# Kernel optimization log

Hardware: AMD Instinct MI355X
Metric: run time of the kernel (lower is better)

## Reference

```python
import jax, jax.numpy as jnp
import numpy as np

HEADS = 16

def setup_inputs() -> dict:
    key = jax.random.key(0)
    ks = jax.random.split(key, 5)
    B, N, D = 2, 2048, 1024
    q = jax.random.normal(ks[0], (B, N, D), dtype=jnp.float32)
    kv = jax.random.normal(ks[1], (B, N, D), dtype=jnp.float32)
    # nn.Linear default init scale ~ 1/sqrt(fan_in); use scaled normals
    s = 1.0 / np.sqrt(D)
    Wq = jax.random.normal(ks[2], (D, D), dtype=jnp.float32) * s
    Wkv = jax.random.normal(ks[3], (D, 2 * D), dtype=jnp.float32) * s
    Wout = jax.random.normal(ks[4], (D, D), dtype=jnp.float32) * s
    return {"q": q, "kv": kv, "Wq": Wq, "Wkv": Wkv, "Wout": Wout}

def reference(q, kv, Wq, Wkv, Wout):
    B, N, D = q.shape
    H = HEADS
    Dh = D // H
    scale = Dh ** -0.5
    # projections (Linear, no bias); weights stored [in, out]
    qp = q @ Wq                      # [B,N,D]
    kvp = kv @ Wkv                   # [B,N,2D]
    kp, vp = kvp[..., :D], kvp[..., D:]
    def split_heads(t):
        return t.reshape(B, N, H, Dh).transpose(0, 2, 1, 3)  # [B,H,N,Dh]
    qh, kh, vh = split_heads(qp), split_heads(kp), split_heads(vp)
    dots = jnp.einsum('bhid,bhjd->bhij', qh, kh) * scale
    # attn_fn = softmax computed in float32, cast back to input dtype
    attn = jax.nn.softmax(dots.astype(jnp.float32), axis=-1).astype(dots.dtype)
    out = jnp.einsum('bhij,bhjd->bhid', attn, vh)
    out = out.transpose(0, 2, 1, 3).reshape(B, N, D)
    return out @ Wout
```

## Files before the change

### kernel.cpp

```cpp
#include <hip/hip_runtime.h>
#include <hip/hip_bf16.h>
#include <stdint.h>

using u16 = unsigned short;
using bf16x8 = __attribute__((ext_vector_type(8))) short;
using bf16x4 = __attribute__((ext_vector_type(4))) short;
using f32x4  = __attribute__((ext_vector_type(4))) float;

__device__ __forceinline__ u16 f2bf(float f) {
  union { float f; uint32_t u; } v; v.f = f;
  uint32_t u = v.u;
  u += 0x7fffu + ((u >> 16) & 1u);
  return (u16)(u >> 16);
}

#define GLOBAL_LOAD_LDS16(gp, lp) \
  __builtin_amdgcn_global_load_lds((const __attribute__((address_space(1))) unsigned int*)(gp), \
                                   (__attribute__((address_space(3))) unsigned int*)(lp), 16, 0, 0)

#define MFMA32(a, b, c) __builtin_amdgcn_mfma_f32_16x16x32_bf16(a, b, c, 0, 0, 0)
#define MFMA16(a, b, c) __builtin_amdgcn_mfma_f32_16x16x16bf16_1k(a, b, c, 0, 0, 0)

__global__ __launch_bounds__(256) void cast2_k(const float4* __restrict__ q,
                                               u16* __restrict__ q16,
                                               const float4* __restrict__ kv,
                                               u16* __restrict__ kv16) {
  int blk = blockIdx.x;
  const float4* in; u16* out; int i;
  if (blk < 4096) { in = q; out = q16; i = blk * 256 + threadIdx.x; }
  else { in = kv; out = kv16; i = (blk - 4096) * 256 + threadIdx.x; }
  float4 f = in[i];
  ushort4 o;
  o.x = f2bf(f.x); o.y = f2bf(f.y); o.z = f2bf(f.z); o.w = f2bf(f.w);
  *(ushort4*)(out + (size_t)i * 4) = o;
}

__global__ __launch_bounds__(256) void prep_w_k(const float* __restrict__ Wq,
                                                const float* __restrict__ Wkv,
                                                const float* __restrict__ Wout,
                                                u16* __restrict__ WqT, u16* __restrict__ WkvT,
                                                u16* __restrict__ WoutT, float qscale) {
  __shared__ float tile[32][33];
  int blk = blockIdx.x;
  const float* in; u16* out; float sc; int idx;
  if (blk < 1024)      { in = Wq;   out = WqT;   sc = qscale; idx = blk; }
  else if (blk < 3072) { in = Wkv;  out = WkvT;  sc = 1.0f;   idx = blk - 1024; }
  else                 { in = Wout; out = WoutT; sc = 1.0f;   idx = blk - 3072; }
  const int K = 1024;
  const int N = (blk >= 1024 && blk < 3072) ? 2048 : 1024;
  int bk = (idx & 31) * 32, bn = (idx >> 5) * 32;
  int tx = threadIdx.x & 31, ty = threadIdx.x >> 5;
#pragma unroll
  for (int i = 0; i < 4; i++) {
    int r = ty * 4 + i;
    tile[r][tx] = in[(size_t)(bk + r) * N + bn + tx];
  }
  __syncthreads();
#pragma unroll
  for (int i = 0; i < 4; i++) {
    int r = ty * 4 + i;
    out[(size_t)(bn + r) * K + bk + tx] = f2bf(tile[tx][r] * sc);
  }
}

template <int BM, bool OUT_F32>
__device__ __forceinline__ void gemm_body(u16* lA, u16* lB,
                                          const u16* __restrict__ A, const u16* __restrict__ BT,
                                          void* __restrict__ Cv, int N, int K, int bm, int bn) {
  const int tid = threadIdx.x;
  const int lane = tid & 63, wave = tid >> 6;
  const int l15 = lane & 15, quad = lane >> 4;
  constexpr int MI = BM / 32;
  const int wm = (wave >> 1) * (BM / 2), wn = (wave & 1) * 64;

  f32x4 acc[MI][4] = {};

  const u16* Abase = A + (size_t)bm * BM * K;
  const u16* Bbase = BT + (size_t)bn * 128 * K;
  const int r0 = tid >> 2, c8 = (tid & 3) * 8;

  u16* lAw = lA + wave * 512;
  u16* lBw = lB + wave * 512;

  for (int k0 = 0; k0 < K; k0 += 32) {
    const u16* Ag = Abase + k0 + (size_t)r0 * K + c8;
    const u16* Bg = Bbase + k0 + (size_t)r0 * K + c8;
#pragma unroll
    for (int t = 0; t < BM / 64; t++)
      GLOBAL_LOAD_LDS16(Ag + (size_t)(t * 64) * K, lAw + t * 2048);
#pragma unroll
    for (int t = 0; t < 2; t++)
      GLOBAL_LOAD_LDS16(Bg + (size_t)(t * 64) * K, lBw + t * 2048);
    __syncthreads();

    bf16x8 aF[MI], bF[4];
#pragma unroll
    for (int mi = 0; mi < MI; mi++)
      aF[mi] = *(const bf16x8*)&lA[(wm + mi * 16 + l15) * 32 + quad * 8];
#pragma unroll
    for (int ni = 0; ni < 4; ni++)
      bF[ni] = *(const bf16x8*)&lB[(wn + ni * 16 + l15) * 32 + quad * 8];
#pragma unroll
    for (int mi = 0; mi < MI; mi++)
#pragma unroll
      for (int ni = 0; ni < 4; ni++)
        acc[mi][ni] = MFMA32(aF[mi], bF[ni], acc[mi][ni]);
    __syncthreads();
  }

  const int col0 = bn * 128 + wn + l15;
  const int rowb = bm * BM + wm + quad * 4;
#pragma unroll
  for (int mi = 0; mi < MI; mi++) {
#pragma unroll
    for (int ni = 0; ni < 4; ni++) {
#pragma unroll
      for (int r = 0; r < 4; r++) {
        int row = rowb + mi * 16 + r;
        int col = col0 + ni * 16;
        float v = acc[mi][ni][r];
        if (OUT_F32) ((float*)Cv)[(size_t)row * N + col] = v;
        else         ((u16*)Cv)[(size_t)row * N + col] = f2bf(v);
      }
    }
  }
}

__global__ __launch_bounds__(256) void proj_k(const u16* __restrict__ q16, const u16* __restrict__ WqT,
                                              u16* __restrict__ qp,
                                              const u16* __restrict__ kv16, const u16* __restrict__ WkvT,
                                              u16* __restrict__ kvp) {
  __shared__ u16 lA[128 * 32];
  __shared__ u16 lB[128 * 32];
  int blk = blockIdx.x;
  if (blk < 256) gemm_body<128, false>(lA, lB, q16, WqT, qp, 1024, 1024, blk >> 3, blk & 7);
  else { int b2 = blk - 256; gemm_body<128, false>(lA, lB, kv16, WkvT, kvp, 2048, 1024, b2 >> 4, b2 & 15); }
}

__global__ __launch_bounds__(256) void gemm_out_k(const u16* __restrict__ A, const u16* __restrict__ BT,
                                                  float* __restrict__ C) {
  __shared__ u16 lA[64 * 32];
  __shared__ u16 lB[128 * 32];
  int blk = blockIdx.x;
  gemm_body<64, true>(lA, lB, A, BT, C, 1024, 1024, blk >> 3, blk & 7);
}

__global__ __launch_bounds__(256) void vt_k(const u16* __restrict__ kvp,
                                            u16* __restrict__ VT) {
  __shared__ u16 lT[64 * 64];
  const int jt = blockIdx.x & 31;
  const int bh = blockIdx.x >> 5;
  const int b = bh >> 4, h = bh & 15;
  const int j0 = jt * 64;
  const int u = threadIdx.x;
  const int su = u >> 3;
  const int sc = (u & 7) * 8;

#pragma unroll
  for (int t = 0; t < 2; t++) {
    int j = su + t * 32;
    int s = (j ^ (j >> 3)) & 7;
    uint4 vv = *(const uint4*)(kvp + (size_t)(b * 2048 + j0 + j) * 2048 + 1024 + h * 64 + sc);
    *(uint4*)&lT[j * 64 + (sc ^ (s << 3))] = vv;
  }
  __syncthreads();

  const int jg = u & 7;
#pragma unroll
  for (int t = 0; t < 2; t++) {
    int d = su + t * 32;
    u16 tmp[8];
#pragma unroll
    for (int i = 0; i < 8; i++) {
      int j = jg * 8 + i;
      int s = (j ^ (j >> 3)) & 7;
      tmp[i] = lT[j * 64 + (d ^ (s << 3))];
    }
    *(uint4*)(VT + ((size_t)bh * 64 + d) * 2048 + j0 + jg * 8) = *(const uint4*)tmp;
  }
}

__global__ __launch_bounds__(256) void flash_attn_k(const u16* __restrict__ qp,
                                                    const u16* __restrict__ kvp,
                                                    const u16* __restrict__ VT,
                                                    u16* __restrict__ attn_out) {
  const int NSEQ = 2048, D = 1024, LDKV = 2048;
  const int mtile = blockIdx.x & 31;
  const int bh = blockIdx.x >> 5;
  const int b = bh >> 4, h = bh & 15;
  const int tid = threadIdx.x;
  const int lane = tid & 63, wave = tid >> 6;
  const int quad = lane >> 4, l15 = lane & 15;

  __shared__ u16 lK[2][128 * 64];
  __shared__ u16 lV[2][64 * 128];

  const u16* Qb  = qp + (size_t)(b * NSEQ + mtile * 64) * D + h * 64;
  const u16* Kb  = kvp + (size_t)(b * NSEQ) * LDKV + h * 64;
  const u16* VTb = VT + (size_t)bh * 64 * 2048;

  bf16x8 qa[2];
#pragma unroll
  for (int ks = 0; ks < 2; ks++)
    qa[ks] = *(const bf16x8*)(Qb + (size_t)(wave * 16 + l15) * D + ks * 32 + quad * 8);

#define STAGE(sel, J0)                                                                   \
  {                                                                                      \
    _Pragma("unroll")                                                                    \
    for (int t = 0; t < 4; t++) {                                                        \
      int g = t * 256 + tid;                                                             \
      int jr = g >> 3;                                                                   \
      int c = (g & 7) ^ (jr & 7);                                                        \
      GLOBAL_LOAD_LDS16(Kb + (size_t)((J0) + jr) * LDKV + c * 8,                         \
                        &lK[sel][wave * 512 + t * 2048]);                                \
    }                                                                                    \
    _Pragma("unroll")                                                                    \
    for (int t = 0; t < 4; t++) {                                                        \
      int g = t * 256 + tid;                                                             \
      int d = g >> 4;                                                                    \
      int c = (g & 15) ^ (d & 7);                                                        \
      GLOBAL_LOAD_LDS16(VTb + (size_t)d * 2048 + (J0) + c * 8,                           \
                        &lV[sel][wave * 512 + t * 2048]);                                \
    }                                                                                    \
  }

  STAGE(0, 0);

  f32x4 oacc[4] = {};
  float rs = 0.f;

  for (int it = 0; it < 16; it++) {
    const int cur = it & 1;
    __syncthreads();
    if (it < 15) STAGE(cur ^ 1, (it + 1) * 128);

    const u16* lKc = lK[cur];
    const u16* lVc = lV[cur];
    f32x4 sacc[8] = {};
#pragma unroll
    for (int ks = 0; ks < 2; ks++)
#pragma unroll
      for (int ni = 0; ni < 8; ni++) {
        int p = ((ks * 4 + quad) ^ (l15 & 7)) * 8;
        bf16x8 kb = *(const bf16x8*)&lKc[(ni * 16 + l15) * 64 + p];
        sacc[ni] = MFMA32(kb, qa[ks], sacc[ni]);
      }

#pragma unroll
    for (int ni = 0; ni < 8; ni++) {
      float p0 = __builtin_amdgcn_exp2f(sacc[ni][0]);
      float p1 = __builtin_amdgcn_exp2f(sacc[ni][1]);
      float p2 = __builtin_amdgcn_exp2f(sacc[ni][2]);
      float p3 = __builtin_amdgcn_exp2f(sacc[ni][3]);
      rs += (p0 + p1) + (p2 + p3);
      union { uint32_t u[2]; bf16x4 v; } pa;
      __hip_bfloat162 w01 = __float22bfloat162_rn(float2{p0, p1});
      __hip_bfloat162 w23 = __float22bfloat162_rn(float2{p2, p3});
      pa.u[0] = *(uint32_t*)&w01;
      pa.u[1] = *(uint32_t*)&w23;
#pragma unroll
      for (int di = 0; di < 4; di++) {
        int p = (((2 * ni + (quad >> 1)) ^ (l15 & 7)) * 8) + (quad & 1) * 4;
        bf16x4 vb = *(const bf16x4*)&lVc[(di * 16 + l15) * 128 + p];
        oacc[di] = MFMA16(pa.v, vb, oacc[di]);
      }
    }
  }

  rs += __shfl_xor(rs, 16, 64);
  rs += __shfl_xor(rs, 32, 64);
  float inv = 1.0f / rs;
  float invq[4];
#pragma unroll
  for (int r = 0; r < 4; r++)
    invq[r] = __shfl(inv, (lane & 48) + ((lane >> 4) << 2) + r, 64);

  u16* Ob = attn_out + (size_t)(b * NSEQ + mtile * 64) * D + h * 64;
#pragma unroll
  for (int di = 0; di < 4; di++)
#pragma unroll
    for (int r = 0; r < 4; r++) {
      float v = oacc[di][r] * invq[r];
      Ob[(size_t)(wave * 16 + quad * 4 + r) * D + di * 16 + l15] = f2bf(v);
    }
}

extern "C" void kernel_launch(void* const* d_in, const int* in_sizes, int n_in,
                              void* d_out, int out_size, void* d_ws, size_t ws_size,
                              hipStream_t stream) {
  const float* q    = (const float*)d_in[0];
  const float* kv   = (const float*)d_in[1];
  const float* Wq   = (const float*)d_in[2];
  const float* Wkv  = (const float*)d_in[3];
  const float* Wout = (const float*)d_in[4];
  float* out = (float*)d_out;

  char* ws = (char*)d_ws;
  const size_t MB = 1024 * 1024;
  u16* q16   = (u16*)(ws + 0);
  u16* kv16  = (u16*)(ws + 8 * MB);
  u16* WqT   = (u16*)(ws + 16 * MB);
  u16* WkvT  = (u16*)(ws + 18 * MB);
  u16* WoutT = (u16*)(ws + 22 * MB);
  u16* qp    = (u16*)(ws + 24 * MB);
  u16* kvp   = (u16*)(ws + 32 * MB);
  u16* attn  = q16;
  u16* VT    = kv16;

  const float qscale = 0.125f * 1.44269504f;

  cast2_k<<<8192, 256, 0, stream>>>((const float4*)q, q16, (const float4*)kv, kv16);
  prep_w_k<<<4096, 256, 0, stream>>>(Wq, Wkv, Wout, WqT, WkvT, WoutT, qscale);

  proj_k<<<768, 256, 0, stream>>>(q16, WqT, qp, kv16, WkvT, kvp);
  vt_k<<<1024, 256, 0, stream>>>(kvp, VT);
  flash_attn_k<<<1024, 256, 0, stream>>>(qp, kvp, VT, attn);
  gemm_out_k<<<512, 256, 0, stream>>>(attn, WoutT, out);
}
```

Baseline: 224.9 us.

## Merge prep kernels, double-buffer GEMM LDS, and process two query tiles per attention block

```diff
diff --git a/kernel.cpp b/kernel.cpp
--- a/kernel.cpp
+++ b/kernel.cpp
@@ -21,33 +21,32 @@
 #define MFMA32(a, b, c) __builtin_amdgcn_mfma_f32_16x16x32_bf16(a, b, c, 0, 0, 0)
 #define MFMA16(a, b, c) __builtin_amdgcn_mfma_f32_16x16x16bf16_1k(a, b, c, 0, 0, 0)
 
-__global__ __launch_bounds__(256) void cast2_k(const float4* __restrict__ q,
-                                               u16* __restrict__ q16,
-                                               const float4* __restrict__ kv,
-                                               u16* __restrict__ kv16) {
-  int blk = blockIdx.x;
-  const float4* in; u16* out; int i;
-  if (blk < 4096) { in = q; out = q16; i = blk * 256 + threadIdx.x; }
-  else { in = kv; out = kv16; i = (blk - 4096) * 256 + threadIdx.x; }
-  float4 f = in[i];
-  ushort4 o;
-  o.x = f2bf(f.x); o.y = f2bf(f.y); o.z = f2bf(f.z); o.w = f2bf(f.w);
-  *(ushort4*)(out + (size_t)i * 4) = o;
-}
-
-__global__ __launch_bounds__(256) void prep_w_k(const float* __restrict__ Wq,
-                                                const float* __restrict__ Wkv,
-                                                const float* __restrict__ Wout,
-                                                u16* __restrict__ WqT, u16* __restrict__ WkvT,
-                                                u16* __restrict__ WoutT, float qscale) {
+__global__ __launch_bounds__(256) void prep_k(const float4* __restrict__ q, u16* __restrict__ q16,
+                                              const float4* __restrict__ kv, u16* __restrict__ kv16,
+                                              const float* __restrict__ Wq,
+                                              const float* __restrict__ Wkv,
+                                              const float* __restrict__ Wout,
+                                              u16* __restrict__ WqT, u16* __restrict__ WkvT,
+                                              u16* __restrict__ WoutT, float qscale) {
   __shared__ float tile[32][33];
   int blk = blockIdx.x;
+  if (blk < 8192) {
+    const float4* in; u16* out; int i;
+    if (blk < 4096) { in = q; out = q16; i = blk * 256 + threadIdx.x; }
+    else { in = kv; out = kv16; i = (blk - 4096) * 256 + threadIdx.x; }
+    float4 f = in[i];
+    ushort4 o;
+    o.x = f2bf(f.x); o.y = f2bf(f.y); o.z = f2bf(f.z); o.w = f2bf(f.w);
+    *(ushort4*)(out + (size_t)i * 4) = o;
+    return;
+  }
+  int b2 = blk - 8192;
   const float* in; u16* out; float sc; int idx;
-  if (blk < 1024)      { in = Wq;   out = WqT;   sc = qscale; idx = blk; }
-  else if (blk < 3072) { in = Wkv;  out = WkvT;  sc = 1.0f;   idx = blk - 1024; }
-  else                 { in = Wout; out = WoutT; sc = 1.0f;   idx = blk - 3072; }
+  if (b2 < 1024)      { in = Wq;   out = WqT;   sc = qscale; idx = b2; }
+  else if (b2 < 3072) { in = Wkv;  out = WkvT;  sc = 1.0f;   idx = b2 - 1024; }
+  else                 { in = Wout; out = WoutT; sc = 1.0f;   idx = b2 - 3072; }
   const int K = 1024;
-  const int N = (blk >= 1024 && blk < 3072) ? 2048 : 1024;
+  const int N = (b2 >= 1024 && b2 < 3072) ? 2048 : 1024;
   int bk = (idx & 31) * 32, bn = (idx >> 5) * 32;
   int tx = threadIdx.x & 31, ty = threadIdx.x >> 5;
 #pragma unroll
@@ -75,38 +74,45 @@
 
   f32x4 acc[MI][4] = {};
 
-  const u16* Abase = A + (size_t)bm * BM * K;
-  const u16* Bbase = BT + (size_t)bn * 128 * K;
   const int r0 = tid >> 2, c8 = (tid & 3) * 8;
-
-  u16* lAw = lA + wave * 512;
-  u16* lBw = lB + wave * 512;
-
-  for (int k0 = 0; k0 < K; k0 += 32) {
-    const u16* Ag = Abase + k0 + (size_t)r0 * K + c8;
-    const u16* Bg = Bbase + k0 + (size_t)r0 * K + c8;
-#pragma unroll
-    for (int t = 0; t < BM / 64; t++)
-      GLOBAL_LOAD_LDS16(Ag + (size_t)(t * 64) * K, lAw + t * 2048);
-#pragma unroll
-    for (int t = 0; t < 2; t++)
-      GLOBAL_LOAD_LDS16(Bg + (size_t)(t * 64) * K, lBw + t * 2048);
+  const u16* Ab = A + (size_t)bm * BM * K + (size_t)r0 * K + c8;
+  const u16* Bb = BT + (size_t)bn * 128 * K + (size_t)r0 * K + c8;
+
+#define STAGE_G(sel, k0)                                                        \
+  {                                                                             \
+    u16* lAw = lA + (sel) * (BM * 32) + wave * 512;                             \
+    u16* lBw = lB + (sel) * (128 * 32) + wave * 512;                            \
+    _Pragma("unroll")                                                           \
+    for (int t = 0; t < BM / 64; t++)                                           \
+      GLOBAL_LOAD_LDS16(Ab + (k0) + (size_t)(t * 64) * K, lAw + t * 2048);      \
+    _Pragma("unroll")                                                           \
+    for (int t = 0; t < 2; t++)                                                 \
+      GLOBAL_LOAD_LDS16(Bb + (k0) + (size_t)(t * 64) * K, lBw + t * 2048);      \
+  }
+
+  STAGE_G(0, 0);
+  const int iters = K >> 5;
+  for (int it = 0; it < iters; it++) {
+    const int cur = it & 1;
     __syncthreads();
-
+    if (it + 1 < iters) STAGE_G(cur ^ 1, (it + 1) * 32);
+
+    const u16* lAc = lA + cur * (BM * 32);
+    const u16* lBc = lB + cur * (128 * 32);
     bf16x8 aF[MI], bF[4];
 #pragma unroll
     for (int mi = 0; mi < MI; mi++)
-      aF[mi] = *(const bf16x8*)&lA[(wm + mi * 16 + l15) * 32 + quad * 8];
+      aF[mi] = *(const bf16x8*)&lAc[(wm + mi * 16 + l15) * 32 + quad * 8];
 #pragma unroll
     for (int ni = 0; ni < 4; ni++)
-      bF[ni] = *(const bf16x8*)&lB[(wn + ni * 16 + l15) * 32 + quad * 8];
+      bF[ni] = *(const bf16x8*)&lBc[(wn + ni * 16 + l15) * 32 + quad * 8];
 #pragma unroll
     for (int mi = 0; mi < MI; mi++)
 #pragma unroll
       for (int ni = 0; ni < 4; ni++)
         acc[mi][ni] = MFMA32(aF[mi], bF[ni], acc[mi][ni]);
-    __syncthreads();
-  }
+  }
+#undef STAGE_G
 
   const int col0 = bn * 128 + wn + l15;
   const int rowb = bm * BM + wm + quad * 4;
@@ -130,8 +136,8 @@
                                               u16* __restrict__ qp,
                                               const u16* __restrict__ kv16, const u16* __restrict__ WkvT,
                                               u16* __restrict__ kvp) {
-  __shared__ u16 lA[128 * 32];
-  __shared__ u16 lB[128 * 32];
+  __shared__ u16 lA[2 * 128 * 32];
+  __shared__ u16 lB[2 * 128 * 32];
   int blk = blockIdx.x;
   if (blk < 256) gemm_body<128, false>(lA, lB, q16, WqT, qp, 1024, 1024, blk >> 3, blk & 7);
   else { int b2 = blk - 256; gemm_body<128, false>(lA, lB, kv16, WkvT, kvp, 2048, 1024, b2 >> 4, b2 & 15); }
@@ -139,8 +145,8 @@
 
 __global__ __launch_bounds__(256) void gemm_out_k(const u16* __restrict__ A, const u16* __restrict__ BT,
                                                   float* __restrict__ C) {
-  __shared__ u16 lA[64 * 32];
-  __shared__ u16 lB[128 * 32];
+  __shared__ u16 lA[2 * 64 * 32];
+  __shared__ u16 lB[2 * 128 * 32];
   int blk = blockIdx.x;
   gemm_body<64, true>(lA, lB, A, BT, C, 1024, 1024, blk >> 3, blk & 7);
 }
@@ -185,8 +191,8 @@
                                                     const u16* __restrict__ VT,
                                                     u16* __restrict__ attn_out) {
   const int NSEQ = 2048, D = 1024, LDKV = 2048;
-  const int mtile = blockIdx.x & 31;
-  const int bh = blockIdx.x >> 5;
+  const int mtile = blockIdx.x & 15;
+  const int bh = blockIdx.x >> 4;
   const int b = bh >> 4, h = bh & 15;
   const int tid = threadIdx.x;
   const int lane = tid & 63, wave = tid >> 6;
@@ -195,14 +201,16 @@
   __shared__ u16 lK[2][128 * 64];
   __shared__ u16 lV[2][64 * 128];
 
-  const u16* Qb  = qp + (size_t)(b * NSEQ + mtile * 64) * D + h * 64;
+  const u16* Qb  = qp + (size_t)(b * NSEQ + mtile * 128) * D + h * 64;
   const u16* Kb  = kvp + (size_t)(b * NSEQ) * LDKV + h * 64;
   const u16* VTb = VT + (size_t)bh * 64 * 2048;
 
-  bf16x8 qa[2];
-#pragma unroll
-  for (int ks = 0; ks < 2; ks++)
-    qa[ks] = *(const bf16x8*)(Qb + (size_t)(wave * 16 + l15) * D + ks * 32 + quad * 8);
+  bf16x8 qa[2][2];
+#pragma unroll
+  for (int qt = 0; qt < 2; qt++)
+#pragma unroll
+    for (int ks = 0; ks < 2; ks++)
+      qa[qt][ks] = *(const bf16x8*)(Qb + (size_t)(qt * 64 + wave * 16 + l15) * D + ks * 32 + quad * 8);
 
 #define STAGE(sel, J0)                                                                   \
   {                                                                                      \
@@ -226,8 +234,8 @@
 
   STAGE(0, 0);
 
-  f32x4 oacc[4] = {};
-  float rs = 0.f;
+  f32x4 oacc[2][4] = {};
+  float rs2[2] = {0.f, 0.f};
 
   for (int it = 0; it < 16; it++) {
     const int cur = it & 1;
@@ -236,53 +244,61 @@
 
     const u16* lKc = lK[cur];
     const u16* lVc = lV[cur];
-    f32x4 sacc[8] = {};
-#pragma unroll
-    for (int ks = 0; ks < 2; ks++)
+#pragma unroll
+    for (int qt = 0; qt < 2; qt++) {
+      f32x4 sacc[8] = {};
+#pragma unroll
+      for (int ks = 0; ks < 2; ks++)
+#pragma unroll
+        for (int ni = 0; ni < 8; ni++) {
+          int p = ((ks * 4 + quad) ^ (l15 & 7)) * 8;
+          bf16x8 kb = *(const bf16x8*)&lKc[(ni * 16 + l15) * 64 + p];
+          sacc[ni] = MFMA32(kb, qa[qt][ks], sacc[ni]);
+        }
+
+      float rs = 0.f;
 #pragma unroll
       for (int ni = 0; ni < 8; ni++) {
-        int p = ((ks * 4 + quad) ^ (l15 & 7)) * 8;
-        bf16x8 kb = *(const bf16x8*)&lKc[(ni * 16 + l15) * 64 + p];
-        sacc[ni] = MFMA32(kb, qa[ks], sacc[ni]);
+        float p0 = __builtin_amdgcn_exp2f(sacc[ni][0]);
+        float p1 = __builtin_amdgcn_exp2f(sacc[ni][1]);
+        float p2 = __builtin_amdgcn_exp2f(sacc[ni][2]);
+        float p3 = __builtin_amdgcn_exp2f(sacc[ni][3]);
+        rs += (p0 + p1) + (p2 + p3);
+        union { uint32_t u[2]; bf16x4 v; } pa;
+        __hip_bfloat162 w01 = __float22bfloat162_rn(float2{p0, p1});
+        __hip_bfloat162 w23 = __float22bfloat162_rn(float2{p2, p3});
+        pa.u[0] = *(uint32_t*)&w01;
+        pa.u[1] = *(uint32_t*)&w23;
+#pragma unroll
+        for (int di = 0; di < 4; di++) {
+          int p = (((2 * ni + (quad >> 1)) ^ (l15 & 7)) * 8) + (quad & 1) * 4;
+          bf16x4 vb = *(const bf16x4*)&lVc[(di * 16 + l15) * 128 + p];
+          oacc[qt][di] = MFMA16(pa.v, vb, oacc[qt][di]);
+        }
       }
-
-#pragma unroll
-    for (int ni = 0; ni < 8; ni++) {
-      float p0 = __builtin_amdgcn_exp2f(sacc[ni][0]);
-      float p1 = __builtin_amdgcn_exp2f(sacc[ni][1]);
-      float p2 = __builtin_amdgcn_exp2f(sacc[ni][2]);
-      float p3 = __builtin_amdgcn_exp2f(sacc[ni][3]);
-      rs += (p0 + p1) + (p2 + p3);
-      union { uint32_t u[2]; bf16x4 v; } pa;
-      __hip_bfloat162 w01 = __float22bfloat162_rn(float2{p0, p1});
-      __hip_bfloat162 w23 = __float22bfloat162_rn(float2{p2, p3});
-      pa.u[0] = *(uint32_t*)&w01;
-      pa.u[1] = *(uint32_t*)&w23;
-#pragma unroll
-      for (int di = 0; di < 4; di++) {
-        int p = (((2 * ni + (quad >> 1)) ^ (l15 & 7)) * 8) + (quad & 1) * 4;
-        bf16x4 vb = *(const bf16x4*)&lVc[(di * 16 + l15) * 128 + p];
-        oacc[di] = MFMA16(pa.v, vb, oacc[di]);
+      rs2[qt] += rs;
+    }
+  }
+
+  u16* Ob = attn_out + (size_t)(b * NSEQ + mtile * 128) * D + h * 64;
+#pragma unroll
+  for (int qt = 0; qt < 2; qt++) {
+    float rs = rs2[qt];
+    rs += __shfl_xor(rs, 16, 64);
+    rs += __shfl_xor(rs, 32, 64);
+    float inv = 1.0f / rs;
+    float invq[4];
+#pragma unroll
+    for (int r = 0; r < 4; r++)
+      invq[r] = __shfl(inv, (lane & 48) + ((lane >> 4) << 2) + r, 64);
+#pragma unroll
+    for (int di = 0; di < 4; di++)
+#pragma unroll
+      for (int r = 0; r < 4; r++) {
+        float v = oacc[qt][di][r] * invq[r];
+        Ob[(size_t)(qt * 64 + wave * 16 + quad * 4 + r) * D + di * 16 + l15] = f2bf(v);
       }
-    }
-  }
-
-  rs += __shfl_xor(rs, 16, 64);
-  rs += __shfl_xor(rs, 32, 64);
-  float inv = 1.0f / rs;
-  float invq[4];
-#pragma unroll
-  for (int r = 0; r < 4; r++)
-    invq[r] = __shfl(inv, (lane & 48) + ((lane >> 4) << 2) + r, 64);
-
-  u16* Ob = attn_out + (size_t)(b * NSEQ + mtile * 64) * D + h * 64;
-#pragma unroll
-  for (int di = 0; di < 4; di++)
-#pragma unroll
-    for (int r = 0; r < 4; r++) {
-      float v = oacc[di][r] * invq[r];
-      Ob[(size_t)(wave * 16 + quad * 4 + r) * D + di * 16 + l15] = f2bf(v);
-    }
+  }
 }
 
 extern "C" void kernel_launch(void* const* d_in, const int* in_sizes, int n_in,
@@ -309,11 +325,10 @@
 
   const float qscale = 0.125f * 1.44269504f;
 
-  cast2_k<<<8192, 256, 0, stream>>>((const float4*)q, q16, (const float4*)kv, kv16);
-  prep_w_k<<<4096, 256, 0, stream>>>(Wq, Wkv, Wout, WqT, WkvT, WoutT, qscale);
-
+  prep_k<<<12288, 256, 0, stream>>>((const float4*)q, q16, (const float4*)kv, kv16,
+                                    Wq, Wkv, Wout, WqT, WkvT, WoutT, qscale);
   proj_k<<<768, 256, 0, stream>>>(q16, WqT, qp, kv16, WkvT, kvp);
   vt_k<<<1024, 256, 0, stream>>>(kvp, VT);
-  flash_attn_k<<<1024, 256, 0, stream>>>(qp, kvp, VT, attn);
+  flash_attn_k<<<512, 256, 0, stream>>>(qp, kvp, VT, attn);
   gemm_out_k<<<512, 256, 0, stream>>>(attn, WoutT, out);
 }
```

Result: slower. 238.4 us (+6.0%).
